# Optimization experiments

Measured on AMD Instinct MI355X. Metric: run time of the kernel, lower is better.

The kernel has to match this reference:

```python
import jax, jax.numpy as jnp
import numpy as np

N = 10000      # nodes
E = 320000     # edges
IN_DIM = 256
HID = 256
EDGE_DIM = 64


def _sage(x, src, dst, w_l, b_l, w_r, n_nodes):
    """PyG SAGEConv (aggr='mean', root_weight=True, normalize=False):
    out_i = lin_l(mean_{j->i} x_j) + lin_r(x_i). Messages flow src->dst."""
    msg = x[src]                                            # [E, F]
    agg = jax.ops.segment_sum(msg, dst, num_segments=n_nodes)
    cnt = jax.ops.segment_sum(jnp.ones((msg.shape[0], 1), x.dtype), dst,
                              num_segments=n_nodes)
    mean = agg / jnp.maximum(cnt, 1.0)                      # [N, F]
    return mean @ w_l.T + b_l + x @ w_r.T                   # [N, HID]


def setup_inputs() -> dict:
    key = jax.random.key(0)
    ks = jax.random.split(key, 13)
    s = 0.02
    return {
        "x": jax.random.normal(ks[0], (N, IN_DIM), dtype=jnp.float32),
        "edge_attr": jax.random.normal(ks[1], (E, EDGE_DIM), dtype=jnp.float32),
        "conv1_wl": jax.random.normal(ks[2], (HID, IN_DIM), dtype=jnp.float32) * s,
        "conv1_bl": jnp.zeros((HID,), dtype=jnp.float32),
        "conv1_wr": jax.random.normal(ks[3], (HID, IN_DIM), dtype=jnp.float32) * s,
        "conv2_wl": jax.random.normal(ks[4], (HID, HID), dtype=jnp.float32) * s,
        "conv2_bl": jnp.zeros((HID,), dtype=jnp.float32),
        "conv2_wr": jax.random.normal(ks[5], (HID, HID), dtype=jnp.float32) * s,
        "mlp_w1": jax.random.normal(ks[6], (HID, 2 * HID + EDGE_DIM), dtype=jnp.float32) * s,
        "mlp_b1": jnp.zeros((HID,), dtype=jnp.float32),
        "mlp_w2": jax.random.normal(ks[7], (1, HID), dtype=jnp.float32) * s,
        "mlp_b2": jnp.zeros((1,), dtype=jnp.float32),
        "edge_index": jax.random.randint(ks[8], (2, E), 0, N, dtype=jnp.int32),
    }


def reference(x, edge_attr, conv1_wl, conv1_bl, conv1_wr,
              conv2_wl, conv2_bl, conv2_wr,
              mlp_w1, mlp_b1, mlp_w2, mlp_b2, edge_index):
    src, dst = edge_index[0], edge_index[1]
    # encode_nodes (dropout is identity in eval mode)
    h = jax.nn.relu(_sage(x, src, dst, conv1_wl, conv1_bl, conv1_wr, N))
    h = _sage(h, src, dst, conv2_wl, conv2_bl, conv2_wr, N)
    # edge_logits: gather endpoints, concat with edge_attr, 2-layer MLP
    feats = jnp.concatenate([h[src], h[dst], edge_attr], axis=1)   # [E, 2H+ED]
    hidden = jax.nn.relu(feats @ mlp_w1.T + mlp_b1)                # [E, H]
    logits = hidden @ mlp_w2.T + mlp_b2                            # [E, 1]
    return logits[:, 0]
```

## Files before the change

kernel.cpp:

```cpp
#include <hip/hip_runtime.h>

#define N_NODES 10000
#define N_EDGES 320000
#define DIM 256
#define ED 64
#define W1_LD 576

__global__ void hist_kernel(const int* __restrict__ dst, int* __restrict__ cnt, int n) {
  int i = blockIdx.x * blockDim.x + threadIdx.x;
  if (i < n) atomicAdd(&cnt[dst[i]], 1);
}

__global__ void scan_kernel(const int* __restrict__ cnt, int* __restrict__ off,
                            int* __restrict__ cursor, int n) {
  __shared__ int wsum[4];
  __shared__ int carry_s;
  int t = threadIdx.x, lane = t & 63, w = t >> 6;
  if (t == 0) carry_s = 0;
  __syncthreads();
  for (int base = 0; base < n; base += 256) {
    int i = base + t;
    int v = (i < n) ? cnt[i] : 0;
    int sc = v;
    #pragma unroll
    for (int s = 1; s < 64; s <<= 1) {
      int u = __shfl_up(sc, s, 64);
      if (lane >= s) sc += u;
    }
    if (lane == 63) wsum[w] = sc;
    __syncthreads();
    int woff = 0, tot = 0;
    #pragma unroll
    for (int j = 0; j < 4; ++j) { int s = wsum[j]; if (j < w) woff += s; tot += s; }
    int excl = sc - v + woff + carry_s;
    if (i < n) { off[i] = excl; cursor[i] = excl; }
    __syncthreads();
    if (t == 0) carry_s += tot;
    __syncthreads();
  }
  if (t == 0) off[n] = carry_s;
}

__global__ void scatter_kernel(const int* __restrict__ src, const int* __restrict__ dst,
                               int* __restrict__ cursor, int* __restrict__ csr_src,
                               int* __restrict__ csr_dst, int* __restrict__ csr_eid, int n) {
  int i = blockIdx.x * blockDim.x + threadIdx.x;
  if (i < n) {
    int d = dst[i];
    int p = atomicAdd(&cursor[d], 1);
    csr_src[p] = src[i];
    csr_dst[p] = d;
    csr_eid[p] = i;
  }
}

template<bool RELU>
__global__ __launch_bounds__(256) void agg_fused_kernel(
    const float* __restrict__ XP,
    const int* __restrict__ off, const int* __restrict__ csr_src,
    const float* __restrict__ bias,
    float* __restrict__ H) {
  int node = blockIdx.x * 4 + (threadIdx.x >> 6);
  int t4 = (threadIdx.x & 63) * 4;
  int beg = off[node], end = off[node + 1];
  float4 root = *(const float4*)&XP[(size_t)node * 512 + 256 + t4];
  float4 bv = *(const float4*)&bias[t4];
  float sx = 0.f, sy = 0.f, sz = 0.f, sw = 0.f;
  int e = beg;
  for (; e + 7 < end; e += 8) {
    int i0 = csr_src[e],   i1 = csr_src[e+1], i2 = csr_src[e+2], i3 = csr_src[e+3];
    int i4 = csr_src[e+4], i5 = csr_src[e+5], i6 = csr_src[e+6], i7 = csr_src[e+7];
    float4 v0 = *(const float4*)&XP[(size_t)i0 * 512 + t4];
    float4 v1 = *(const float4*)&XP[(size_t)i1 * 512 + t4];
    float4 v2 = *(const float4*)&XP[(size_t)i2 * 512 + t4];
    float4 v3 = *(const float4*)&XP[(size_t)i3 * 512 + t4];
    float4 v4 = *(const float4*)&XP[(size_t)i4 * 512 + t4];
    float4 v5 = *(const float4*)&XP[(size_t)i5 * 512 + t4];
    float4 v6 = *(const float4*)&XP[(size_t)i6 * 512 + t4];
    float4 v7 = *(const float4*)&XP[(size_t)i7 * 512 + t4];
    sx += ((v0.x + v1.x) + (v2.x + v3.x)) + ((v4.x + v5.x) + (v6.x + v7.x));
    sy += ((v0.y + v1.y) + (v2.y + v3.y)) + ((v4.y + v5.y) + (v6.y + v7.y));
    sz += ((v0.z + v1.z) + (v2.z + v3.z)) + ((v4.z + v5.z) + (v6.z + v7.z));
    sw += ((v0.w + v1.w) + (v2.w + v3.w)) + ((v4.w + v5.w) + (v6.w + v7.w));
  }
  for (; e < end; ++e) {
    int s = csr_src[e];
    float4 v = *(const float4*)&XP[(size_t)s * 512 + t4];
    sx += v.x; sy += v.y; sz += v.z; sw += v.w;
  }
  int deg = end - beg;
  float inv = 1.0f / (float)(deg > 0 ? deg : 1);
  float4 r;
  r.x = sx * inv + bv.x + root.x;
  r.y = sy * inv + bv.y + root.y;
  r.z = sz * inv + bv.z + root.z;
  r.w = sw * inv + bv.w + root.w;
  if (RELU) {
    r.x = fmaxf(r.x, 0.f); r.y = fmaxf(r.y, 0.f);
    r.z = fmaxf(r.z, 0.f); r.w = fmaxf(r.w, 0.f);
  }
  *(float4*)&H[(size_t)node * 256 + t4] = r;
}

__global__ __launch_bounds__(256) void gemm_kernel(
    const float* __restrict__ A,
    const float* __restrict__ Wlo, const float* __restrict__ Whi,
    const float* __restrict__ bias, float* __restrict__ C,
    int nrows, int ldw, int split) {
  __shared__ float As[32][64];
  __shared__ float Bs[32][64];
  int t = threadIdx.x;
  int tx = t & 15, ty = t >> 4;
  int row0 = blockIdx.x * 64;
  int col0 = blockIdx.y * 64;

  const float* W = Wlo;
  int obase = col0;
  if (col0 >= split) { W = Whi; obase = col0 - split; }

  float acc[4][4];
  #pragma unroll
  for (int i = 0; i < 4; ++i)
    #pragma unroll
    for (int j = 0; j < 4; ++j) acc[i][j] = 0.f;

  for (int kt = 0; kt < 8; ++kt) {
    int kb = kt * 32;
    __syncthreads();
    #pragma unroll
    for (int i = 0; i < 2; ++i) {
      int idx = i * 256 + t;
      int m = idx >> 3;
      int kq = idx & 7;
      int row = row0 + m;
      float4 v = make_float4(0.f, 0.f, 0.f, 0.f);
      if (row < nrows) v = *(const float4*)&A[(size_t)row * 256 + kb + kq * 4];
      As[kq * 4 + 0][m] = v.x; As[kq * 4 + 1][m] = v.y;
      As[kq * 4 + 2][m] = v.z; As[kq * 4 + 3][m] = v.w;
    }
    #pragma unroll
    for (int i = 0; i < 2; ++i) {
      int idx = i * 256 + t;
      int o = idx >> 3;
      int kq = idx & 7;
      float4 v = *(const float4*)&W[(size_t)(obase + o) * ldw + kb + kq * 4];
      Bs[kq * 4 + 0][o] = v.x; Bs[kq * 4 + 1][o] = v.y;
      Bs[kq * 4 + 2][o] = v.z; Bs[kq * 4 + 3][o] = v.w;
    }
    __syncthreads();
    #pragma unroll 8
    for (int k = 0; k < 32; ++k) {
      float4 a0 = *(const float4*)&As[k][ty * 4];
      float4 b0 = *(const float4*)&Bs[k][tx * 4];
      float a[4] = {a0.x, a0.y, a0.z, a0.w};
      float b[4] = {b0.x, b0.y, b0.z, b0.w};
      #pragma unroll
      for (int i = 0; i < 4; ++i)
        #pragma unroll
        for (int j = 0; j < 4; ++j)
          acc[i][j] += a[i] * b[j];
    }
  }
  float4 bv = make_float4(0.f, 0.f, 0.f, 0.f);
  if (bias && col0 < split) bv = *(const float4*)&bias[col0 + tx * 4];
  #pragma unroll
  for (int i = 0; i < 4; ++i) {
    int row = row0 + ty * 4 + i;
    if (row < nrows) {
      float4 o4;
      o4.x = acc[i][0] + bv.x; o4.y = acc[i][1] + bv.y;
      o4.z = acc[i][2] + bv.z; o4.w = acc[i][3] + bv.w;
      *(float4*)&C[(size_t)row * 512 + col0 + tx * 4] = o4;
    }
  }
}

#define EB 128
__global__ __launch_bounds__(512, 6) void edge_kernel(
    const float* __restrict__ edge_attr,
    const int* __restrict__ csr_src, const int* __restrict__ csr_dst,
    const int* __restrict__ csr_eid,
    const float* __restrict__ PQ,
    const float* __restrict__ mlp_w1,
    const float* __restrict__ w2,
    const float* __restrict__ b2,
    float* __restrict__ out) {
  __shared__ float w_lds[64][64];
  __shared__ float ea_lds[64][EB];

  int t = threadIdx.x;
  int e0 = blockIdx.x * EB;
  {
    int e_l = t >> 2, q = t & 3;
    int eid = csr_eid[e0 + e_l];
    const float* ep = &edge_attr[(size_t)eid * ED + q * 16];
    #pragma unroll
    for (int j = 0; j < 4; ++j) {
      float4 v = *(const float4*)&ep[j * 4];
      int k = q * 16 + j * 4;
      ea_lds[k + 0][e_l] = v.x; ea_lds[k + 1][e_l] = v.y;
      ea_lds[k + 2][e_l] = v.z; ea_lds[k + 3][e_l] = v.w;
    }
  }
  int c = t & 15, r = t >> 4;
  const float* pbase[4];
  const float* qbase[4];
  int eout[4];
  #pragma unroll
  for (int i = 0; i < 4; ++i) {
    int el = e0 + r * 4 + i;
    pbase[i] = &PQ[(size_t)csr_src[el] * 512 + c * 4];
    qbase[i] = &PQ[(size_t)csr_dst[el] * 512 + 256 + c * 4];
    eout[i] = csr_eid[el];
  }
  float logit[4] = {0.f, 0.f, 0.f, 0.f};
  float4 pf[4], qf[4];
  #pragma unroll
  for (int i = 0; i < 4; ++i) {
    pf[i] = *(const float4*)&pbase[i][0];
    qf[i] = *(const float4*)&qbase[i][0];
  }

  for (int chunk = 0; chunk < 4; ++chunk) {
    #pragma unroll
    for (int i = 0; i < 2; ++i) {
      int idx = i * 512 + t;
      int o = idx & 63;
      int kq = idx >> 6;
      float4 v = *(const float4*)&mlp_w1[(size_t)(chunk * 64 + o) * W1_LD + 512 + kq * 4];
      w_lds[kq * 4 + 0][o] = v.x; w_lds[kq * 4 + 1][o] = v.y;
      w_lds[kq * 4 + 2][o] = v.z; w_lds[kq * 4 + 3][o] = v.w;
    }
    __syncthreads();
    float acc[4][4];
    #pragma unroll
    for (int i = 0; i < 4; ++i)
      #pragma unroll
      for (int j = 0; j < 4; ++j) acc[i][j] = 0.f;
    #pragma unroll 8
    for (int k = 0; k < 64; ++k) {
      float4 a = *(const float4*)&ea_lds[k][r * 4];
      float4 wv4 = *(const float4*)&w_lds[k][c * 4];
      float av[4] = {a.x, a.y, a.z, a.w};
      float wv[4] = {wv4.x, wv4.y, wv4.z, wv4.w};
      #pragma unroll
      for (int i = 0; i < 4; ++i)
        #pragma unroll
        for (int j = 0; j < 4; ++j)
          acc[i][j] += av[i] * wv[j];
    }
    float4 w2v = *(const float4*)&w2[chunk * 64 + c * 4];
    #pragma unroll
    for (int i = 0; i < 4; ++i) {
      float s0 = fmaxf(acc[i][0] + pf[i].x + qf[i].x, 0.f);
      float s1 = fmaxf(acc[i][1] + pf[i].y + qf[i].y, 0.f);
      float s2 = fmaxf(acc[i][2] + pf[i].z + qf[i].z, 0.f);
      float s3 = fmaxf(acc[i][3] + pf[i].w + qf[i].w, 0.f);
      logit[i] += s0 * w2v.x + s1 * w2v.y + s2 * w2v.z + s3 * w2v.w;
    }
    if (chunk < 3) {
      int coff = (chunk + 1) * 64;
      #pragma unroll
      for (int i = 0; i < 4; ++i) {
        pf[i] = *(const float4*)&pbase[i][coff];
        qf[i] = *(const float4*)&qbase[i][coff];
      }
      __syncthreads();
    }
  }
  #pragma unroll
  for (int m = 1; m < 16; m <<= 1) {
    #pragma unroll
    for (int i = 0; i < 4; ++i) logit[i] += __shfl_xor(logit[i], m, 64);
  }
  if (c == 0) {
    float bb = b2[0];
    #pragma unroll
    for (int i = 0; i < 4; ++i) out[eout[i]] = logit[i] + bb;
  }
}

static inline size_t alignup(size_t x) { return (x + 255) & ~(size_t)255; }

extern "C" void kernel_launch(void* const* d_in, const int* in_sizes, int n_in,
                              void* d_out, int out_size, void* d_ws, size_t ws_size,
                              hipStream_t stream) {
  const float* x    = (const float*)d_in[0];
  const float* ea   = (const float*)d_in[1];
  const float* c1wl = (const float*)d_in[2];
  const float* c1bl = (const float*)d_in[3];
  const float* c1wr = (const float*)d_in[4];
  const float* c2wl = (const float*)d_in[5];
  const float* c2bl = (const float*)d_in[6];
  const float* c2wr = (const float*)d_in[7];
  const float* w1   = (const float*)d_in[8];
  const float* b1   = (const float*)d_in[9];
  const float* w2   = (const float*)d_in[10];
  const float* b2   = (const float*)d_in[11];
  const int*   ei   = (const int*)d_in[12];
  const int* src = ei;
  const int* dst = ei + N_EDGES;
  float* out = (float*)d_out;

  char* p = (char*)d_ws;
  size_t o = 0;
  int* cnt      = (int*)(p + o); o += alignup(N_NODES * 4);
  int* off      = (int*)(p + o); o += alignup((N_NODES + 1) * 4);
  int* cursor   = (int*)(p + o); o += alignup(N_NODES * 4);
  int* csr_src  = (int*)(p + o); o += alignup(N_EDGES * 4);
  int* csr_dst  = (int*)(p + o); o += alignup(N_EDGES * 4);
  int* csr_eid  = (int*)(p + o); o += alignup(N_EDGES * 4);
  float* XP     = (float*)(p + o); o += alignup((size_t)N_NODES * 512 * 4);
  float* h      = (float*)(p + o); o += alignup((size_t)N_NODES * 256 * 4);
  float* PQ     = (float*)(p + o); o += alignup((size_t)N_NODES * 512 * 4);

  hipMemsetAsync(cnt, 0, N_NODES * 4, stream);
  hist_kernel<<<(N_EDGES + 255) / 256, 256, 0, stream>>>(dst, cnt, N_EDGES);
  scan_kernel<<<1, 256, 0, stream>>>(cnt, off, cursor, N_NODES);
  scatter_kernel<<<(N_EDGES + 255) / 256, 256, 0, stream>>>(
      src, dst, cursor, csr_src, csr_dst, csr_eid, N_EDGES);

  dim3 ggrid((N_NODES + 63) / 64, 8);

  gemm_kernel<<<ggrid, 256, 0, stream>>>(x, c1wl, c1wr, nullptr, XP, N_NODES, DIM, 256);
  agg_fused_kernel<true><<<N_NODES / 4, 256, 0, stream>>>(XP, off, csr_src, c1bl, h);

  gemm_kernel<<<ggrid, 256, 0, stream>>>(h, c2wl, c2wr, nullptr, XP, N_NODES, DIM, 256);
  agg_fused_kernel<false><<<N_NODES / 4, 256, 0, stream>>>(XP, off, csr_src, c2bl, h);

  gemm_kernel<<<ggrid, 256, 0, stream>>>(h, w1, w1 + 256, b1, PQ, N_NODES, W1_LD, 256);

  edge_kernel<<<N_EDGES / EB, 512, 0, stream>>>(
      ea, csr_src, csr_dst, csr_eid, PQ, w1, w2, b2, out);
}
```

Before: 678.3 us.

## Rewrite scan as per-thread chunks, enlarge GEMM row tile, shrink edge blocks

The single-block scan now gives each thread a contiguous chunk of 40 counts and does one block-wide scan, replacing a 40-iteration loop that synchronised on every step. The node GEMM tile doubles to 128 rows per block, with each thread holding 8x4 accumulators for more reuse of the weight tile. The edge kernel drops to 64 edges per block with 256 threads, so there are more, smaller blocks. The costs are more registers per GEMM thread, fewer GEMM blocks, and a large register array in the scan.

After: 586.3 us. 1.16x faster.

```diff
diff --git a/kernel.cpp b/kernel.cpp
--- a/kernel.cpp
+++ b/kernel.cpp
@@ -11,34 +11,38 @@
   if (i < n) atomicAdd(&cnt[dst[i]], 1);
 }
 
+#define SCAN_CH 40
 __global__ void scan_kernel(const int* __restrict__ cnt, int* __restrict__ off,
                             int* __restrict__ cursor, int n) {
   __shared__ int wsum[4];
-  __shared__ int carry_s;
   int t = threadIdx.x, lane = t & 63, w = t >> 6;
-  if (t == 0) carry_s = 0;
+  int base = t * SCAN_CH;
+  int loc[SCAN_CH];
+  int tot = 0;
+  #pragma unroll
+  for (int j = 0; j < SCAN_CH; ++j) {
+    int i = base + j;
+    loc[j] = tot;
+    tot += (i < n) ? cnt[i] : 0;
+  }
+  int sc = tot;
+  #pragma unroll
+  for (int s = 1; s < 64; s <<= 1) {
+    int u = __shfl_up(sc, s, 64);
+    if (lane >= s) sc += u;
+  }
+  if (lane == 63) wsum[w] = sc;
   __syncthreads();
-  for (int base = 0; base < n; base += 256) {
-    int i = base + t;
-    int v = (i < n) ? cnt[i] : 0;
-    int sc = v;
-    #pragma unroll
-    for (int s = 1; s < 64; s <<= 1) {
-      int u = __shfl_up(sc, s, 64);
-      if (lane >= s) sc += u;
-    }
-    if (lane == 63) wsum[w] = sc;
-    __syncthreads();
-    int woff = 0, tot = 0;
-    #pragma unroll
-    for (int j = 0; j < 4; ++j) { int s = wsum[j]; if (j < w) woff += s; tot += s; }
-    int excl = sc - v + woff + carry_s;
-    if (i < n) { off[i] = excl; cursor[i] = excl; }
-    __syncthreads();
-    if (t == 0) carry_s += tot;
-    __syncthreads();
-  }
-  if (t == 0) off[n] = carry_s;
+  int woff = 0;
+  #pragma unroll
+  for (int j = 0; j < 4; ++j) { int s = wsum[j]; if (j < w) woff += s; }
+  int tbase = sc - tot + woff;
+  #pragma unroll
+  for (int j = 0; j < SCAN_CH; ++j) {
+    int i = base + j;
+    if (i < n) { int v = tbase + loc[j]; off[i] = v; cursor[i] = v; }
+    else if (i == n) { off[n] = tbase + loc[j]; }
+  }
 }
 
 __global__ void scatter_kernel(const int* __restrict__ src, const int* __restrict__ dst,
@@ -107,20 +111,20 @@
     const float* __restrict__ Wlo, const float* __restrict__ Whi,
     const float* __restrict__ bias, float* __restrict__ C,
     int nrows, int ldw, int split) {
-  __shared__ float As[32][64];
+  __shared__ float As[32][128];
   __shared__ float Bs[32][64];
   int t = threadIdx.x;
   int tx = t & 15, ty = t >> 4;
-  int row0 = blockIdx.x * 64;
+  int row0 = blockIdx.x * 128;
   int col0 = blockIdx.y * 64;
 
   const float* W = Wlo;
   int obase = col0;
   if (col0 >= split) { W = Whi; obase = col0 - split; }
 
-  float acc[4][4];
-  #pragma unroll
-  for (int i = 0; i < 4; ++i)
+  float acc[8][4];
+  #pragma unroll
+  for (int i = 0; i < 8; ++i)
     #pragma unroll
     for (int j = 0; j < 4; ++j) acc[i][j] = 0.f;
 
@@ -128,7 +132,7 @@
     int kb = kt * 32;
     __syncthreads();
     #pragma unroll
-    for (int i = 0; i < 2; ++i) {
+    for (int i = 0; i < 4; ++i) {
       int idx = i * 256 + t;
       int m = idx >> 3;
       int kq = idx & 7;
@@ -151,11 +155,12 @@
     #pragma unroll 8
     for (int k = 0; k < 32; ++k) {
       float4 a0 = *(const float4*)&As[k][ty * 4];
+      float4 a1 = *(const float4*)&As[k][ty * 4 + 64];
       float4 b0 = *(const float4*)&Bs[k][tx * 4];
-      float a[4] = {a0.x, a0.y, a0.z, a0.w};
+      float a[8] = {a0.x, a0.y, a0.z, a0.w, a1.x, a1.y, a1.z, a1.w};
       float b[4] = {b0.x, b0.y, b0.z, b0.w};
       #pragma unroll
-      for (int i = 0; i < 4; ++i)
+      for (int i = 0; i < 8; ++i)
         #pragma unroll
         for (int j = 0; j < 4; ++j)
           acc[i][j] += a[i] * b[j];
@@ -164,8 +169,9 @@
   float4 bv = make_float4(0.f, 0.f, 0.f, 0.f);
   if (bias && col0 < split) bv = *(const float4*)&bias[col0 + tx * 4];
   #pragma unroll
-  for (int i = 0; i < 4; ++i) {
-    int row = row0 + ty * 4 + i;
+  for (int i = 0; i < 8; ++i) {
+    int m = ty * 4 + (i & 3) + (i >> 2) * 64;
+    int row = row0 + m;
     if (row < nrows) {
       float4 o4;
       o4.x = acc[i][0] + bv.x; o4.y = acc[i][1] + bv.y;
@@ -175,8 +181,8 @@
   }
 }
 
-#define EB 128
-__global__ __launch_bounds__(512, 6) void edge_kernel(
+#define EB 64
+__global__ __launch_bounds__(256, 4) void edge_kernel(
     const float* __restrict__ edge_attr,
     const int* __restrict__ csr_src, const int* __restrict__ csr_dst,
     const int* __restrict__ csr_eid,
@@ -223,8 +229,8 @@
 
   for (int chunk = 0; chunk < 4; ++chunk) {
     #pragma unroll
-    for (int i = 0; i < 2; ++i) {
-      int idx = i * 512 + t;
+    for (int i = 0; i < 4; ++i) {
+      int idx = i * 256 + t;
       int o = idx & 63;
       int kq = idx >> 6;
       float4 v = *(const float4*)&mlp_w1[(size_t)(chunk * 64 + o) * W1_LD + 512 + kq * 4];
@@ -320,7 +326,7 @@
   scatter_kernel<<<(N_EDGES + 255) / 256, 256, 0, stream>>>(
       src, dst, cursor, csr_src, csr_dst, csr_eid, N_EDGES);
 
-  dim3 ggrid((N_NODES + 63) / 64, 8);
+  dim3 ggrid((N_NODES + 127) / 128, 8);
 
   gemm_kernel<<<ggrid, 256, 0, stream>>>(x, c1wl, c1wr, nullptr, XP, N_NODES, DIM, 256);
   agg_fused_kernel<true><<<N_NODES / 4, 256, 0, stream>>>(XP, off, csr_src, c1bl, h);
@@ -330,6 +336,6 @@
 
   gemm_kernel<<<ggrid, 256, 0, stream>>>(h, w1, w1 + 256, b1, PQ, N_NODES, W1_LD, 256);
 
-  edge_kernel<<<N_EDGES / EB, 512, 0, stream>>>(
+  edge_kernel<<<N_EDGES / EB, 256, 0, stream>>>(
       ea, csr_src, csr_dst, csr_eid, PQ, w1, w2, b2, out);
 }
```
